# Kernel optimization log

Hardware: AMD Instinct MI355X
Metric: run time of the kernel (lower is better)

Reference implementation:

```python
import jax, jax.numpy as jnp
import numpy as np

GROUPS = 8
EPS = 1e-5
V, CIN, COUT, K, TDIM, B = 49152, 128, 256, 8, 256, 1
E = V * 9


def group_norm(x, gamma, beta):
    # x: [B, V, C]; torch GroupNorm semantics: normalize over (pixels, channels-in-group)
    b, v, c = x.shape
    xg = x.reshape(b, v, GROUPS, c // GROUPS)
    mu = xg.mean(axis=(1, 3), keepdims=True)
    var = xg.var(axis=(1, 3), keepdims=True)
    xg = (xg - mu) * jax.lax.rsqrt(var + EPS)
    return xg.reshape(b, v, c) * gamma + beta


def cheb_conv(x, row, col, vals, w):
    # x: [B, V, C]; w: [K, C, F]; Chebyshev recurrence on sparse Laplacian
    b, v, c = x.shape
    k = w.shape[0]
    xt = x.transpose(1, 0, 2).reshape(v, b * c)  # [V, B*C]

    def spmv(z):  # sparse L @ z via scatter-add
        return jnp.zeros_like(z).at[row].add(vals[:, None] * z[col])

    terms = [xt]
    if k > 1:
        terms.append(spmv(xt))
    for _ in range(k - 2):
        terms.append(2.0 * spmv(terms[-1]) - terms[-2])
    t = jnp.stack(terms).reshape(k, v, b, c)  # [K, V, B, C]
    return jnp.einsum('kvbc,kcf->bvf', t, w)  # [B, V, F]


def setup_inputs() -> dict:
    key = jax.random.key(0)
    ks = jax.random.split(key, 12)
    return {
        'x': jax.random.normal(ks[0], (B, V, CIN), jnp.float32),
        'time_emb': jax.random.normal(ks[1], (B, TDIM), jnp.float32),
        'row': jax.random.randint(ks[2], (E,), 0, V),
        'col': jax.random.randint(ks[3], (E,), 0, V),
        'vals': jax.random.normal(ks[4], (E,), jnp.float32) * 0.1,
        'w_res': jax.random.normal(ks[5], (K, CIN, COUT), jnp.float32) * 0.05,
        'w1': jax.random.normal(ks[6], (K, CIN, COUT), jnp.float32) * 0.05,
        'w2': jax.random.normal(ks[7], (K, COUT, COUT), jnp.float32) * 0.05,
        'g1': jnp.ones((CIN,), jnp.float32),
        'b1': jnp.zeros((CIN,), jnp.float32),
        'g2': jnp.ones((COUT,), jnp.float32),
        'b2': jnp.zeros((COUT,), jnp.float32),
        'wt': jax.random.normal(ks[8], (TDIM, COUT), jnp.float32) * 0.05,
        'bt': jnp.zeros((COUT,), jnp.float32),
    }


def reference(x, time_emb, row, col, vals, w_res, w1, w2, g1, b1, g2, b2, wt, bt):
    # conv_res (in_channels != out_channels), pooling = identity
    res = cheb_conv(x, row, col, vals, w_res)
    # block1: conv(silu(group_norm(x)))
    h = cheb_conv(jax.nn.silu(group_norm(x, g1, b1)), row, col, vals, w1)
    # time embedding: SiLU -> Linear -> broadcast over pixels
    h = h + (jax.nn.silu(time_emb) @ wt + bt)[:, None, :]
    # block2
    h = cheb_conv(jax.nn.silu(group_norm(h, g2, b2)), row, col, vals, w2)
    return h + res
```

## Files before the change

kernel.cpp:

```cpp
#include <hip/hip_runtime.h>
#include <cstddef>

#define V_N 49152
#define E_N 442368
#define GEPS 1e-5f
#define CO 256
#define TD 256

typedef _Float16 h16;
typedef _Float16 h8v __attribute__((ext_vector_type(8)));
typedef _Float16 h4v __attribute__((ext_vector_type(4)));
typedef float f4v __attribute__((ext_vector_type(4)));

__device__ __forceinline__ void gload_lds16(const void* g, void* l) {
    __builtin_amdgcn_global_load_lds(
        (const __attribute__((address_space(1))) unsigned int*)g,
        (__attribute__((address_space(3))) unsigned int*)l, 16, 0, 0);
}

__global__ void count_edges(const int* __restrict__ row, int* __restrict__ cnt) {
    int e = blockIdx.x * blockDim.x + threadIdx.x;
    if (e < E_N) atomicAdd(&cnt[row[e]], 1);
}

__global__ void scan_rowptr(int* __restrict__ cnt, int* __restrict__ rowptr) {
    __shared__ int part[1024];
    const int CHUNK = V_N / 1024;
    int t = threadIdx.x;
    int base = t * CHUNK;
    int s = 0;
    for (int i = 0; i < CHUNK; ++i) s += cnt[base + i];
    part[t] = s;
    __syncthreads();
    for (int off = 1; off < 1024; off <<= 1) {
        int v = part[t];
        int add = (t >= off) ? part[t - off] : 0;
        __syncthreads();
        part[t] = v + add;
        __syncthreads();
    }
    int run = (t == 0) ? 0 : part[t - 1];
    for (int i = 0; i < CHUNK; ++i) {
        int c = cnt[base + i];
        rowptr[base + i] = run;
        cnt[base + i] = run;
        run += c;
    }
    if (t == 1023) rowptr[V_N] = run;
}

__global__ void fill_csr(const int* __restrict__ row, const int* __restrict__ col,
                         const float* __restrict__ vals, int* __restrict__ cursor,
                         int2* __restrict__ ep) {
    int e = blockIdx.x * blockDim.x + threadIdx.x;
    if (e < E_N) {
        int r = row[e];
        int slot = atomicAdd(&cursor[r], 1);
        ep[slot] = make_int2(col[e], __float_as_int(vals[e]));
    }
}

__global__ void wprep(const float* __restrict__ w, h16* __restrict__ wt, int KC) {
    __shared__ float t[16][17];
    int kc = blockIdx.x * 16 + threadIdx.y;
    int f = blockIdx.y * 16 + threadIdx.x;
    t[threadIdx.y][threadIdx.x] = w[(size_t)kc * CO + f];
    __syncthreads();
    int fo = blockIdx.y * 16 + threadIdx.y;
    int kco = blockIdx.x * 16 + threadIdx.x;
    wt[(size_t)fo * KC + kco] = (h16)t[threadIdx.x][threadIdx.y];
}

template <int C>
__global__ void gn_stats2(const float* __restrict__ x, const float* __restrict__ tvec,
                          float* __restrict__ part) {
    __shared__ float ls[8], lss[8];
    int t = threadIdx.x;
    if (t < 8) { ls[t] = 0.f; lss[t] = 0.f; }
    __syncthreads();
    const int total4 = V_N * (C / 4);
    const int cmask = (C / 4) - 1;
    const int stride = gridDim.x * blockDim.x;
    int i0 = blockIdx.x * blockDim.x + t;
    const int c4 = i0 & cmask;
    float t0 = 0.f, t1 = 0.f, t2 = 0.f, t3 = 0.f;
    if (tvec) {
        t0 = tvec[c4 * 4 + 0]; t1 = tvec[c4 * 4 + 1];
        t2 = tvec[c4 * 4 + 2]; t3 = tvec[c4 * 4 + 3];
    }
    float s = 0.f, ss = 0.f;
    for (int i = i0; i < total4; i += stride) {
        float4 v = ((const float4*)x)[i];
        v.x += t0; v.y += t1; v.z += t2; v.w += t3;
        s  += v.x + v.y + v.z + v.w;
        ss += v.x * v.x + v.y * v.y + v.z * v.z + v.w * v.w;
    }
    constexpr int GL = (C == 128) ? 4 : 8;
#pragma unroll
    for (int off = 1; off < GL; off <<= 1) {
        s  += __shfl_xor(s, off);
        ss += __shfl_xor(ss, off);
    }
    int lane = t & 63;
    if ((lane & (GL - 1)) == 0) {
        int g = c4 >> ((C == 128) ? 2 : 3);
        atomicAdd(&ls[g], s);
        atomicAdd(&lss[g], ss);
    }
    __syncthreads();
    if (t < 16) part[blockIdx.x * 16 + t] = (t < 8) ? ls[t] : lss[t - 8];
}

#define GN_BLOCKS 512

__global__ void gn_reduce(const float* __restrict__ part, float* __restrict__ stats,
                          int nb) {
    __shared__ float acc[16];
    int t = threadIdx.x;
    if (t < 16) acc[t] = 0.f;
    __syncthreads();
    int idx = t & 15;
    float s = 0.f;
    for (int j = t >> 4; j < nb; j += 16) s += part[j * 16 + idx];
    atomicAdd(&acc[idx], s);
    __syncthreads();
    if (t < 16) stats[t] = acc[t];
}

__global__ void gn1_apply(const float* __restrict__ x, const float* __restrict__ stats,
                          const float* __restrict__ gamma, const float* __restrict__ beta,
                          h16* __restrict__ dst, int ldT) {
    const float Ng = (float)V_N * 16.f;
    const int total4 = V_N * 32;
    for (int i = blockIdx.x * blockDim.x + threadIdx.x; i < total4;
         i += gridDim.x * blockDim.x) {
        int c4 = i & 31;
        int v = i >> 5;
        float4 xv = ((const float4*)x)[i];
        float in[4] = {xv.x, xv.y, xv.z, xv.w};
        h4v o, oc;
#pragma unroll
        for (int j = 0; j < 4; ++j) {
            int c = c4 * 4 + j;
            int g = c >> 4;
            float mu = stats[g] / Ng;
            float var = stats[8 + g] / Ng - mu * mu;
            float rs = rsqrtf(var + GEPS);
            float y = (in[j] - mu) * rs * gamma[c] + beta[c];
            y = y / (1.f + expf(-y));
            o[j] = (h16)y;
            oc[j] = (h16)in[j];
        }
        size_t base = (size_t)v * ldT + c4 * 4;
        *(h4v*)&dst[base] = o;
        *(h4v*)&dst[base + 128] = oc;
    }
}

__global__ void gn2_apply(const float* __restrict__ x, const float* __restrict__ tvec,
                          const float* __restrict__ stats, const float* __restrict__ gamma,
                          const float* __restrict__ beta, h16* __restrict__ dst, int ldT) {
    const float Ng = (float)V_N * 32.f;
    const int total4 = V_N * 64;
    for (int i = blockIdx.x * blockDim.x + threadIdx.x; i < total4;
         i += gridDim.x * blockDim.x) {
        int c4 = i & 63;
        int v = i >> 6;
        float4 xv = ((const float4*)x)[i];
        float in[4] = {xv.x, xv.y, xv.z, xv.w};
        h4v o;
#pragma unroll
        for (int j = 0; j < 4; ++j) {
            int c = c4 * 4 + j;
            int g = c >> 5;
            float mu = stats[g] / Ng;
            float var = stats[8 + g] / Ng - mu * mu;
            float rs = rsqrtf(var + GEPS);
            float val = in[j] + tvec[c];
            float y = (val - mu) * rs * gamma[c] + beta[c];
            y = y / (1.f + expf(-y));
            o[j] = (h16)y;
        }
        *(h4v*)&dst[(size_t)v * ldT + c4 * 4] = o;
    }
}

__global__ void time_mlp(const float* __restrict__ te, const float* __restrict__ wt,
                         const float* __restrict__ bt, float* __restrict__ tvec) {
    __shared__ float s[TD];
    int f = threadIdx.x;
    float v = te[f];
    s[f] = v / (1.f + expf(-v));
    __syncthreads();
    float acc = bt[f];
    for (int t = 0; t < TD; ++t) acc += s[t] * wt[t * CO + f];
    tvec[f] = acc;
}

template <bool RECUR>
__global__ void spmv2(const int* __restrict__ rowptr, const int2* __restrict__ ep,
                      const h16* __restrict__ zb, const h16* __restrict__ pb,
                      h16* __restrict__ db, int ldT) {
    int wid = threadIdx.x >> 6, lane = threadIdx.x & 63;
    int v = blockIdx.x * 4 + wid;
    int s = rowptr[v], e = rowptr[v + 1];
    int half = lane >> 5, hl = lane & 31;
    float acc[8];
#pragma unroll
    for (int i = 0; i < 8; ++i) acc[i] = 0.f;
    for (int j = s; j < e; j += 4) {
        int j0 = j + half, j1 = j + half + 2;
        int2 p0 = ep[(j0 < e) ? j0 : (e - 1)];
        int2 p1 = ep[(j1 < e) ? j1 : (e - 1)];
        float v0 = (j0 < e) ? __int_as_float(p0.y) : 0.f;
        float v1 = (j1 < e) ? __int_as_float(p1.y) : 0.f;
        h8v z0 = *(const h8v*)&zb[(size_t)p0.x * ldT + hl * 8];
        h8v z1 = *(const h8v*)&zb[(size_t)p1.x * ldT + hl * 8];
#pragma unroll
        for (int i = 0; i < 8; ++i) acc[i] += v0 * (float)z0[i];
#pragma unroll
        for (int i = 0; i < 8; ++i) acc[i] += v1 * (float)z1[i];
    }
#pragma unroll
    for (int i = 0; i < 8; ++i) acc[i] += __shfl_xor(acc[i], 32);
    if (half == 0) {
        size_t base = (size_t)v * ldT + hl * 8;
        h8v o;
        if (RECUR) {
            h8v pv = *(const h8v*)&pb[base];
#pragma unroll
            for (int i = 0; i < 8; ++i) o[i] = (h16)(2.f * acc[i] - (float)pv[i]);
        } else {
#pragma unroll
            for (int i = 0; i < 8; ++i) o[i] = (h16)acc[i];
        }
        *(h8v*)&db[base] = o;
    }
}

template <int MODE, bool DUAL>
__global__ __launch_bounds__(256, 3) void gemm_f16(
    const h16* __restrict__ A, int lda, const h16* __restrict__ Wt,
    const h16* __restrict__ Wt2, int ldw, int wofs, int KC, int ksh,
    const float* __restrict__ bias, float* __restrict__ out,
    float* __restrict__ out2) {
    __shared__ h16 As[64 * 32];
    __shared__ h16 Bs[256 * 32];
    if (DUAL && blockIdx.y) { A += 128; Wt = Wt2; out = out2; }
    const int tid = threadIdx.x;
    const int wid = tid >> 6, lane = tid & 63;
    const int m0 = blockIdx.x * 64;
    const int fr = lane & 15, fq = lane >> 4;
    const int rl = lane >> 2;
    const int qs = (lane & 3) ^ ((lane >> 3) & 3);
    const int kmsk = (1 << ksh) - 1;
    const h16* Wb = Wt + wofs;

    f4v acc[4][4];
#pragma unroll
    for (int i = 0; i < 4; ++i)
#pragma unroll
        for (int n = 0; n < 4; ++n) acc[i][n] = (f4v){0.f, 0.f, 0.f, 0.f};

    for (int k0 = 0; k0 < KC; k0 += 32) {
        int ca = (((k0 >> ksh) << 8) | (k0 & kmsk)) + qs * 8;
        int cb = k0 + qs * 8;
        __syncthreads();
        gload_lds16(A + (size_t)(m0 + wid * 16 + rl) * lda + ca, &As[(wid * 16) * 32]);
#pragma unroll
        for (int j = 0; j < 4; ++j) {
            int rbase = wid * 64 + j * 16;
            gload_lds16(Wb + (size_t)(rbase + rl) * ldw + cb, &Bs[rbase * 32]);
        }
        __syncthreads();
        const int slot = (fq ^ ((fr >> 1) & 3)) * 8;
        h8v af[4], bf[4];
#pragma unroll
        for (int i = 0; i < 4; ++i)
            af[i] = *(const h8v*)&As[(i * 16 + fr) * 32 + slot];
#pragma unroll
        for (int n = 0; n < 4; ++n)
            bf[n] = *(const h8v*)&Bs[(wid * 64 + n * 16 + fr) * 32 + slot];
#pragma unroll
        for (int i = 0; i < 4; ++i)
#pragma unroll
            for (int n = 0; n < 4; ++n)
                acc[i][n] = __builtin_amdgcn_mfma_f32_16x16x32_f16(af[i], bf[n],
                                                                   acc[i][n], 0, 0, 0);
    }
#pragma unroll
    for (int i = 0; i < 4; ++i)
#pragma unroll
        for (int n = 0; n < 4; ++n)
#pragma unroll
            for (int rr = 0; rr < 4; ++rr) {
                int row = m0 + i * 16 + fq * 4 + rr;
                int col = wid * 64 + n * 16 + fr;
                size_t idx = (size_t)row * CO + col;
                if (MODE == 0) out[idx] = acc[i][n][rr];
                else if (MODE == 1) out[idx] += acc[i][n][rr];
                else out[idx] = bias[idx] + acc[i][n][rr];
            }
}

static void chain_spmv(hipStream_t s, int chunk, int k0, int kend, h16* terms, int ldT,
                       const int* rp, const int2* ep) {
    for (int k = (k0 == 0 ? 1 : k0); k < kend; ++k) {
        const h16* zb = terms + ((k - 1) % chunk) * 256;
        h16* db = terms + (k % chunk) * 256;
        if (k == 1) {
            spmv2<false><<<V_N / 4, 256, 0, s>>>(rp, ep, zb, nullptr, db, ldT);
        } else {
            const h16* pb = terms + ((k - 2) % chunk) * 256;
            spmv2<true><<<V_N / 4, 256, 0, s>>>(rp, ep, zb, pb, db, ldT);
        }
    }
}

extern "C" void kernel_launch(void* const* d_in, const int* in_sizes, int n_in,
                              void* d_out, int out_size, void* d_ws, size_t ws_size,
                              hipStream_t stream) {
    const float* x    = (const float*)d_in[0];
    const float* te   = (const float*)d_in[1];
    const int*   row  = (const int*)d_in[2];
    const int*   col  = (const int*)d_in[3];
    const float* vals = (const float*)d_in[4];
    const float* wres = (const float*)d_in[5];
    const float* w1   = (const float*)d_in[6];
    const float* w2   = (const float*)d_in[7];
    const float* g1   = (const float*)d_in[8];
    const float* b1   = (const float*)d_in[9];
    const float* g2   = (const float*)d_in[10];
    const float* b2   = (const float*)d_in[11];
    const float* wt   = (const float*)d_in[12];
    const float* bt   = (const float*)d_in[13];
    float* out = (float*)d_out;

    const size_t slot_b = (size_t)V_N * 256 * 2;
    const size_t res_b  = (size_t)V_N * 256 * 4;
    const size_t csr_b  = (size_t)(V_N + V_N + 1) * 4 + (size_t)E_N * 8;
    const size_t wt_b   = (size_t)(1024 + 2048 + 1024) * CO * 2;
    const size_t misc_b = 8192 + (size_t)GN_BLOCKS * 16 * 4;
    auto need = [&](int ch) { return (size_t)ch * slot_b + res_b + csr_b + wt_b + misc_b; };
    int chunk = (ws_size >= need(4)) ? 4 : 2;
    if (ws_size < need(2)) return;
    const int ldT = chunk * 256;

    char* p = (char*)d_ws;
    h16* terms = (h16*)p;              p += (size_t)chunk * slot_b;
    float* resbuf = (float*)p;         p += res_b;
    h16* w1t = (h16*)p;                p += (size_t)1024 * CO * 2;
    h16* w2t = (h16*)p;                p += (size_t)2048 * CO * 2;
    h16* wrt = (h16*)p;                p += (size_t)1024 * CO * 2;
    int* cnt = (int*)p;                p += (size_t)V_N * 4;
    int* rp  = (int*)p;                p += (size_t)(V_N + 1) * 4;
    int2* ep = (int2*)p;               p += (size_t)E_N * 8;
    float* stats = (float*)p;          p += 64;
    float* tv = (float*)p;             p += 1024;
    float* gpart = (float*)p;          p += (size_t)GN_BLOCKS * 16 * 4;

    hipMemsetAsync(cnt, 0, V_N * sizeof(int), stream);
    count_edges<<<E_N / 256, 256, 0, stream>>>(row, cnt);
    scan_rowptr<<<1, 1024, 0, stream>>>(cnt, rp);
    fill_csr<<<E_N / 256, 256, 0, stream>>>(row, col, vals, cnt, ep);

    wprep<<<dim3(1024 / 16, 16), dim3(16, 16), 0, stream>>>(w1, w1t, 1024);
    wprep<<<dim3(2048 / 16, 16), dim3(16, 16), 0, stream>>>(w2, w2t, 2048);
    wprep<<<dim3(1024 / 16, 16), dim3(16, 16), 0, stream>>>(wres, wrt, 1024);

    time_mlp<<<1, 256, 0, stream>>>(te, wt, bt, tv);

    gn_stats2<128><<<GN_BLOCKS, 256, 0, stream>>>(x, nullptr, gpart);
    gn_reduce<<<1, 256, 0, stream>>>(gpart, stats, GN_BLOCKS);
    gn1_apply<<<2048, 256, 0, stream>>>(x, stats, g1, b1, terms, ldT);

    for (int k0 = 0; k0 < 8; k0 += chunk) {
        int kend = (k0 + chunk < 8) ? k0 + chunk : 8;
        chain_spmv(stream, chunk, k0, kend, terms, ldT, rp, ep);
        int KC = (kend - k0) * 128;
        dim3 g(V_N / 64, 2);
        if (k0 == 0)
            gemm_f16<0, true><<<g, 256, 0, stream>>>(terms, ldT, w1t, wrt, 1024,
                                                     k0 * 128, KC, 7, nullptr, out, resbuf);
        else
            gemm_f16<1, true><<<g, 256, 0, stream>>>(terms, ldT, w1t, wrt, 1024,
                                                     k0 * 128, KC, 7, nullptr, out, resbuf);
    }

    gn_stats2<256><<<GN_BLOCKS, 256, 0, stream>>>(out, tv, gpart);
    gn_reduce<<<1, 256, 0, stream>>>(gpart, stats, GN_BLOCKS);
    gn2_apply<<<2048, 256, 0, stream>>>(out, tv, stats, g2, b2, terms, ldT);

    for (int k0 = 0; k0 < 8; k0 += chunk) {
        int kend = (k0 + chunk < 8) ? k0 + chunk : 8;
        chain_spmv(stream, chunk, k0, kend, terms, ldT, rp, ep);
        int KC = (kend - k0) * 256;
        dim3 g(V_N / 64);
        if (k0 == 0)
            gemm_f16<2, false><<<g, 256, 0, stream>>>(terms, ldT, w2t, nullptr, 2048,
                                                      0, KC, 8, resbuf, out, nullptr);
        else
            gemm_f16<1, false><<<g, 256, 0, stream>>>(terms, ldT, w2t, nullptr, 2048,
                                                      k0 * 256, KC, 8, nullptr, out, nullptr);
    }
}
```

Baseline: 882.7 us.

## Pad CSR rows to multiples of eight and vectorize SpMV edge loads

The row-pointer scan now rounds each row's edge count up to a multiple of eight, and the edge array is zero-filled so padded slots have column 0 and value 0. This lets the SpMV loop read edges as int4 pairs and process four edges per half-wave per iteration with no bounds checks. The intent is to cut per-edge branch and index overhead and to issue more independent gathers at once. The GEMM now stages two 32-wide K slices per barrier pair, halving the number of syncs, at the cost of doubled LDS that may lower occupancy. The Chebyshev chunk size may also grow to 8 when the workspace allows, and the extra memset adds a little setup time.

```diff
diff --git a/kernel.cpp b/kernel.cpp
--- a/kernel.cpp
+++ b/kernel.cpp
@@ -3,6 +3,7 @@
 
 #define V_N 49152
 #define E_N 442368
+#define E_PAD 786432
 #define GEPS 1e-5f
 #define CO 256
 #define TD 256
@@ -29,7 +30,7 @@
     int t = threadIdx.x;
     int base = t * CHUNK;
     int s = 0;
-    for (int i = 0; i < CHUNK; ++i) s += cnt[base + i];
+    for (int i = 0; i < CHUNK; ++i) s += (cnt[base + i] + 7) & ~7;
     part[t] = s;
     __syncthreads();
     for (int off = 1; off < 1024; off <<= 1) {
@@ -44,7 +45,7 @@
         int c = cnt[base + i];
         rowptr[base + i] = run;
         cnt[base + i] = run;
-        run += c;
+        run += (c + 7) & ~7;
     }
     if (t == 1023) rowptr[V_N] = run;
 }
@@ -208,18 +209,21 @@
     float acc[8];
 #pragma unroll
     for (int i = 0; i < 8; ++i) acc[i] = 0.f;
-    for (int j = s; j < e; j += 4) {
-        int j0 = j + half, j1 = j + half + 2;
-        int2 p0 = ep[(j0 < e) ? j0 : (e - 1)];
-        int2 p1 = ep[(j1 < e) ? j1 : (e - 1)];
-        float v0 = (j0 < e) ? __int_as_float(p0.y) : 0.f;
-        float v1 = (j1 < e) ? __int_as_float(p1.y) : 0.f;
-        h8v z0 = *(const h8v*)&zb[(size_t)p0.x * ldT + hl * 8];
-        h8v z1 = *(const h8v*)&zb[(size_t)p1.x * ldT + hl * 8];
-#pragma unroll
-        for (int i = 0; i < 8; ++i) acc[i] += v0 * (float)z0[i];
-#pragma unroll
-        for (int i = 0; i < 8; ++i) acc[i] += v1 * (float)z1[i];
+    const int4* e4 = (const int4*)(ep + s);
+    int n2 = (e - s) >> 1;
+    for (int i = 2 * half; i < n2; i += 4) {
+        int4 a = e4[i];
+        int4 b = e4[i + 1];
+        h8v z0 = *(const h8v*)&zb[(size_t)a.x * ldT + hl * 8];
+        h8v z1 = *(const h8v*)&zb[(size_t)a.z * ldT + hl * 8];
+        h8v z2 = *(const h8v*)&zb[(size_t)b.x * ldT + hl * 8];
+        h8v z3 = *(const h8v*)&zb[(size_t)b.z * ldT + hl * 8];
+        float v0 = __int_as_float(a.y), v1 = __int_as_float(a.w);
+        float v2 = __int_as_float(b.y), v3 = __int_as_float(b.w);
+#pragma unroll
+        for (int k = 0; k < 8; ++k)
+            acc[k] += v0 * (float)z0[k] + v1 * (float)z1[k] +
+                      v2 * (float)z2[k] + v3 * (float)z3[k];
     }
 #pragma unroll
     for (int i = 0; i < 8; ++i) acc[i] += __shfl_xor(acc[i], 32);
@@ -244,8 +248,8 @@
     const h16* __restrict__ Wt2, int ldw, int wofs, int KC, int ksh,
     const float* __restrict__ bias, float* __restrict__ out,
     float* __restrict__ out2) {
-    __shared__ h16 As[64 * 32];
-    __shared__ h16 Bs[256 * 32];
+    __shared__ h16 As[2][64 * 32];
+    __shared__ h16 Bs[2][256 * 32];
     if (DUAL && blockIdx.y) { A += 128; Wt = Wt2; out = out2; }
     const int tid = threadIdx.x;
     const int wid = tid >> 6, lane = tid & 63;
@@ -262,31 +266,39 @@
 #pragma unroll
         for (int n = 0; n < 4; ++n) acc[i][n] = (f4v){0.f, 0.f, 0.f, 0.f};
 
-    for (int k0 = 0; k0 < KC; k0 += 32) {
-        int ca = (((k0 >> ksh) << 8) | (k0 & kmsk)) + qs * 8;
-        int cb = k0 + qs * 8;
+    for (int k0 = 0; k0 < KC; k0 += 64) {
         __syncthreads();
-        gload_lds16(A + (size_t)(m0 + wid * 16 + rl) * lda + ca, &As[(wid * 16) * 32]);
-#pragma unroll
-        for (int j = 0; j < 4; ++j) {
-            int rbase = wid * 64 + j * 16;
-            gload_lds16(Wb + (size_t)(rbase + rl) * ldw + cb, &Bs[rbase * 32]);
+#pragma unroll
+        for (int t = 0; t < 2; ++t) {
+            int kk = k0 + t * 32;
+            int ca = (((kk >> ksh) << 8) | (kk & kmsk)) + qs * 8;
+            int cb = kk + qs * 8;
+            gload_lds16(A + (size_t)(m0 + wid * 16 + rl) * lda + ca,
+                        &As[t][(wid * 16) * 32]);
+#pragma unroll
+            for (int j = 0; j < 4; ++j) {
+                int rbase = wid * 64 + j * 16;
+                gload_lds16(Wb + (size_t)(rbase + rl) * ldw + cb, &Bs[t][rbase * 32]);
+            }
         }
         __syncthreads();
         const int slot = (fq ^ ((fr >> 1) & 3)) * 8;
-        h8v af[4], bf[4];
-#pragma unroll
-        for (int i = 0; i < 4; ++i)
-            af[i] = *(const h8v*)&As[(i * 16 + fr) * 32 + slot];
-#pragma unroll
-        for (int n = 0; n < 4; ++n)
-            bf[n] = *(const h8v*)&Bs[(wid * 64 + n * 16 + fr) * 32 + slot];
-#pragma unroll
-        for (int i = 0; i < 4; ++i)
+#pragma unroll
+        for (int t = 0; t < 2; ++t) {
+            h8v af[4], bf[4];
+#pragma unroll
+            for (int i = 0; i < 4; ++i)
+                af[i] = *(const h8v*)&As[t][(i * 16 + fr) * 32 + slot];
 #pragma unroll
             for (int n = 0; n < 4; ++n)
-                acc[i][n] = __builtin_amdgcn_mfma_f32_16x16x32_f16(af[i], bf[n],
-                                                                   acc[i][n], 0, 0, 0);
+                bf[n] = *(const h8v*)&Bs[t][(wid * 64 + n * 16 + fr) * 32 + slot];
+#pragma unroll
+            for (int i = 0; i < 4; ++i)
+#pragma unroll
+                for (int n = 0; n < 4; ++n)
+                    acc[i][n] = __builtin_amdgcn_mfma_f32_16x16x32_f16(af[i], bf[n],
+                                                                       acc[i][n], 0, 0, 0);
+        }
     }
 #pragma unroll
     for (int i = 0; i < 4; ++i)
@@ -338,11 +350,11 @@
 
     const size_t slot_b = (size_t)V_N * 256 * 2;
     const size_t res_b  = (size_t)V_N * 256 * 4;
-    const size_t csr_b  = (size_t)(V_N + V_N + 1) * 4 + (size_t)E_N * 8;
+    const size_t csr_b  = (size_t)(V_N + V_N + 1) * 4 + (size_t)E_PAD * 8;
     const size_t wt_b   = (size_t)(1024 + 2048 + 1024) * CO * 2;
     const size_t misc_b = 8192 + (size_t)GN_BLOCKS * 16 * 4;
     auto need = [&](int ch) { return (size_t)ch * slot_b + res_b + csr_b + wt_b + misc_b; };
-    int chunk = (ws_size >= need(4)) ? 4 : 2;
+    int chunk = (ws_size >= need(8)) ? 8 : (ws_size >= need(4)) ? 4 : 2;
     if (ws_size < need(2)) return;
     const int ldT = chunk * 256;
 
@@ -354,12 +366,13 @@
     h16* wrt = (h16*)p;                p += (size_t)1024 * CO * 2;
     int* cnt = (int*)p;                p += (size_t)V_N * 4;
     int* rp  = (int*)p;                p += (size_t)(V_N + 1) * 4;
-    int2* ep = (int2*)p;               p += (size_t)E_N * 8;
+    int2* ep = (int2*)p;               p += (size_t)E_PAD * 8;
     float* stats = (float*)p;          p += 64;
     float* tv = (float*)p;             p += 1024;
     float* gpart = (float*)p;          p += (size_t)GN_BLOCKS * 16 * 4;
 
     hipMemsetAsync(cnt, 0, V_N * sizeof(int), stream);
+    hipMemsetAsync(ep, 0, (size_t)E_PAD * 8, stream);
     count_edges<<<E_N / 256, 256, 0, stream>>>(row, cnt);
     scan_rowptr<<<1, 1024, 0, stream>>>(cnt, rp);
     fill_csr<<<E_N / 256, 256, 0, stream>>>(row, col, vals, cnt, ep);
```

New measurement: 894.8 us. About the same (+1.4%).
